# Performance work log

Measured on AMD Instinct MI355X. Metric: run time of the kernel, lower is better.

Reference implementation:

```python
import jax, jax.numpy as jnp
import numpy as np

N_NODES = 100000
N_EDGES = 600000
IN_FEATS = 128
OUT_FEATS = 128
BN_EPS = 1e-5


def setup_inputs() -> dict:
    key = jax.random.key(0)
    ks = jax.random.split(key, 8)
    x = jax.random.normal(ks[0], (N_NODES, IN_FEATS), dtype=jnp.float32)
    edge_index = jax.random.randint(ks[1], (2, N_EDGES), 0, N_NODES, dtype=jnp.int64)
    # GCNConv linear weight (no bias in lin), bias added after aggregation
    W = jax.random.normal(ks[2], (IN_FEATS, OUT_FEATS), dtype=jnp.float32) / np.sqrt(IN_FEATS)
    b = jax.random.normal(ks[3], (OUT_FEATS,), dtype=jnp.float32) * 0.01
    # BatchNorm affine params
    gamma = jnp.ones((OUT_FEATS,), dtype=jnp.float32)
    beta = jnp.zeros((OUT_FEATS,), dtype=jnp.float32)
    # residual Linear: y = x @ W_res + b_res (W_res stored [in, out])
    W_res = jax.random.normal(ks[4], (IN_FEATS, OUT_FEATS), dtype=jnp.float32) / np.sqrt(IN_FEATS)
    b_res = jax.random.normal(ks[5], (OUT_FEATS,), dtype=jnp.float32) * 0.01
    return {"x": x, "edge_index": edge_index, "W": W, "b": b,
            "gamma": gamma, "beta": beta, "W_res": W_res, "b_res": b_res}


def _gcn_forward(x, edge_index, W, b, gamma, beta, W_res, b_res):
    n = x.shape[0]
    # --- GCNConv (PyG defaults): add self-loops, symmetric normalization ---
    loops = jnp.arange(n, dtype=edge_index.dtype)
    row = jnp.concatenate([edge_index[0], loops])  # source nodes
    col = jnp.concatenate([edge_index[1], loops])  # destination nodes
    deg = jax.ops.segment_sum(jnp.ones_like(col, dtype=x.dtype), col, num_segments=n)
    dinv = jax.lax.rsqrt(deg)  # deg >= 1 thanks to self-loops
    norm = dinv[row] * dinv[col]  # [E+N]
    h = x @ W  # [N, out]
    msg = h[row] * norm[:, None]  # gather + scale, [E+N, out]
    agg = jax.ops.segment_sum(msg, col, num_segments=n) + b  # scatter-add + bias
    # --- ReLU + BatchNorm (training mode, biased variance) ---
    r = jax.nn.relu(agg)
    mean = jnp.mean(r, axis=0)
    var = jnp.mean(jnp.square(r - mean), axis=0)
    bn = gamma * (r - mean) * jax.lax.rsqrt(var + BN_EPS) + beta
    # --- residual dense path ---
    res = x @ W_res + b_res
    return bn + res


def reference(x, edge_index, W, b, gamma, beta, W_res, b_res):
    return _gcn_forward(x, edge_index, W, b, gamma, beta, W_res, b_res)
```

## Files before the change

### kernel.cpp

```cpp
#include <hip/hip_runtime.h>

#define NN 100000
#define NE 600000
#define F  128
#define BN_EPS 1e-5f
#define TM 128
#define TK 32

typedef short bf8 __attribute__((ext_vector_type(8)));
typedef float f32x4 __attribute__((ext_vector_type(4)));

__device__ __forceinline__ unsigned short bf16_rne(float x) {
    unsigned u = __float_as_uint(x);
    return (unsigned short)((u + 0x7FFFu + ((u >> 16) & 1u)) >> 16);
}
__device__ __forceinline__ void split_bf16(float x, unsigned short& h, unsigned short& l) {
    unsigned short hh = bf16_rne(x);
    float hf = __uint_as_float(((unsigned)hh) << 16);
    h = hh;
    l = bf16_rne(x - hf);
}

__global__ void k_init(const unsigned* __restrict__ ei, int* __restrict__ flag,
                       int* __restrict__ cnt, float* __restrict__ colsum, float* __restrict__ colsq)
{
    int i = blockIdx.x * 256 + threadIdx.x;
    if (i <= NN) cnt[i] = 0;
    if (i < F) { colsum[i] = 0.f; colsq[i] = 0.f; }
    if (blockIdx.x == 0) {
        __shared__ int any;
        if (threadIdx.x == 0) any = 0;
        __syncthreads();
        unsigned v = ei[2 * threadIdx.x + 1];
        if (v != 0u) atomicOr(&any, 1);
        __syncthreads();
        if (threadIdx.x == 0) *flag = (any == 0) ? 1 : 0;
    }
}

__global__ void k_count(const void* __restrict__ ei, const int* __restrict__ flag, int* __restrict__ cnt)
{
    int e = blockIdx.x * 256 + threadIdx.x;
    if (e >= NE) return;
    int col;
    if (*flag) col = (int)((const long long*)ei)[NE + e];
    else       col = ((const int*)ei)[NE + e];
    atomicAdd(&cnt[col], 1);
}

__global__ void k_bsum(const int* __restrict__ cnt, int* __restrict__ bsum)
{
    __shared__ int s[256];
    int b = blockIdx.x, t = threadIdx.x;
    int i = b * 256 + t;
    s[t] = (i <= NN) ? cnt[i] : 0;
    __syncthreads();
    for (int o = 128; o > 0; o >>= 1) {
        if (t < o) s[t] += s[t + o];
        __syncthreads();
    }
    if (t == 0) bsum[b] = s[0];
}

__global__ void k_bscan(const int* __restrict__ bsum, int* __restrict__ bbase)
{
    __shared__ int s[512];
    int t = threadIdx.x;
    int v = (t < 391) ? bsum[t] : 0;
    s[t] = v;
    __syncthreads();
    for (int o = 1; o < 512; o <<= 1) {
        int tmp = (t >= o) ? s[t - o] : 0;
        __syncthreads();
        s[t] += tmp;
        __syncthreads();
    }
    if (t < 391) bbase[t] = s[t] - v;
}

__global__ void k_offsets(const int* __restrict__ cnt, const int* __restrict__ bbase,
                          int* __restrict__ off, int* __restrict__ cur,
                          float* __restrict__ dinv)
{
    __shared__ int s[256];
    int b = blockIdx.x, t = threadIdx.x;
    int i = b * 256 + t;
    int v = (i <= NN) ? cnt[i] : 0;
    s[t] = v;
    __syncthreads();
    for (int o = 1; o < 256; o <<= 1) {
        int tmp = (t >= o) ? s[t - o] : 0;
        __syncthreads();
        s[t] += tmp;
        __syncthreads();
    }
    int excl = s[t] - v + bbase[b];
    if (i <= NN) {
        off[i] = excl;
        if (i < NN) {
            cur[i] = excl;
            float d = (float)(v + 1);
            float r = rsqrtf(d);
            r = r * (1.5f - 0.5f * d * r * r);
            dinv[i] = r;
        }
    }
}

__global__ void k_place(const void* __restrict__ ei, const int* __restrict__ flag,
                        int* __restrict__ cur, int* __restrict__ csr)
{
    int e = blockIdx.x * 256 + threadIdx.x;
    if (e >= NE) return;
    int row, col;
    if (*flag) {
        row = (int)((const long long*)ei)[e];
        col = (int)((const long long*)ei)[NE + e];
    } else {
        row = ((const int*)ei)[e];
        col = ((const int*)ei)[NE + e];
    }
    int slot = atomicAdd(&cur[col], 1);
    csr[slot] = row;
}

__global__ __launch_bounds__(256) void k_agg(const float* __restrict__ x, const float* __restrict__ dinv,
                                             const int* __restrict__ off, const int* __restrict__ csr,
                                             float* __restrict__ aggx,
                                             const float* __restrict__ W, const float* __restrict__ Wr,
                                             unsigned short* __restrict__ wprep)
{
    int node = blockIdx.x * 4 + (threadIdx.x >> 6);
    int lane = threadIdx.x & 63;
    int sub  = lane & 31;
    int half = lane >> 5;
    float ax = 0.f, ay = 0.f, az = 0.f, aw = 0.f;
    int e0 = off[node], e1 = off[node + 1];
    int e = e0 + half;
    for (; e + 2 < e1; e += 4) {
        int r0 = csr[e], r1 = csr[e + 2];
        float s0 = dinv[r0], s1 = dinv[r1];
        float4 u0 = ((const float4*)(x + (size_t)r0 * F))[sub];
        float4 u1 = ((const float4*)(x + (size_t)r1 * F))[sub];
        ax = fmaf(u0.x, s0, ax); ay = fmaf(u0.y, s0, ay);
        az = fmaf(u0.z, s0, az); aw = fmaf(u0.w, s0, aw);
        ax = fmaf(u1.x, s1, ax); ay = fmaf(u1.y, s1, ay);
        az = fmaf(u1.z, s1, az); aw = fmaf(u1.w, s1, aw);
    }
    for (; e < e1; e += 2) {
        int r = csr[e]; float s = dinv[r];
        float4 u = ((const float4*)(x + (size_t)r * F))[sub];
        ax = fmaf(u.x, s, ax); ay = fmaf(u.y, s, ay);
        az = fmaf(u.z, s, az); aw = fmaf(u.w, s, aw);
    }
    ax += __shfl_xor(ax, 32); ay += __shfl_xor(ay, 32);
    az += __shfl_xor(az, 32); aw += __shfl_xor(aw, 32);
    if (half == 0) {
        float di = dinv[node];
        float4 v = ((const float4*)(x + (size_t)node * F))[sub];
        float4 o;
        o.x = (fmaf(v.x, di, ax)) * di;
        o.y = (fmaf(v.y, di, ay)) * di;
        o.z = (fmaf(v.z, di, az)) * di;
        o.w = (fmaf(v.w, di, aw)) * di;
        ((float4*)(aggx + (size_t)node * F))[sub] = o;
    }
    if (blockIdx.x < 16) {
        int t = blockIdx.x * 256 + threadIdx.x;
        int wl  = t & 63;
        int nf  = (t >> 6) & 7;
        int c   = (t >> 9) & 3;
        int typ = t >> 11;
        const float* wsrc = typ ? Wr : W;
        int col = nf * 16 + (wl & 15);
        int k0  = c * 32 + (wl >> 4) * 8;
        unsigned short hi[8], lo[8];
#pragma unroll
        for (int j = 0; j < 8; ++j)
            split_bf16(wsrc[(size_t)(k0 + j) * F + col], hi[j], lo[j]);
        unsigned short* dst = wprep + (size_t)t * 16;
#pragma unroll
        for (int j = 0; j < 8; ++j) { dst[j] = hi[j]; dst[8 + j] = lo[j]; }
    }
}

__global__ __launch_bounds__(256, 2) void k_gemm2(
    float* __restrict__ A, const float* __restrict__ X,
    const unsigned short* __restrict__ wprep,
    const float* __restrict__ bias, const float* __restrict__ biasr,
    float* __restrict__ out, float* __restrict__ colsum, float* __restrict__ colsq)
{
    __shared__ unsigned short Ahi[TM][40];
    __shared__ unsigned short Alo[TM][40];
    __shared__ float sstat[256];

    const int tid  = threadIdx.x;
    const int type = blockIdx.y;
    const int r0   = blockIdx.x * TM;
    const float* __restrict__ src = type ? X : (const float*)A;

    const int lane = tid & 63;
    const int wv = tid >> 6;
    const int wr = wv >> 1;
    const int wc = wv & 1;
    const int l15 = lane & 15;
    const int lq4 = lane >> 4;
    const int k0  = lq4 * 8;

    const int arow  = tid >> 3;
    const int aslot = (tid & 7) << 2;

    float4 ra[4];
#pragma unroll
    for (int it = 0; it < 4; ++it) {
        int gr = r0 + arow + it * 32;
        ra[it] = make_float4(0.f, 0.f, 0.f, 0.f);
        if (gr < NN) ra[it] = *(const float4*)(src + (size_t)gr * F + aslot);
    }
    bf8 bhi[4], blo[4];
#pragma unroll
    for (int n = 0; n < 4; ++n) {
        int entry = ((type * 4 + 0) * 8 + wc * 4 + n) * 64 + lane;
        const bf8* pb = (const bf8*)(wprep + (size_t)entry * 16);
        bhi[n] = pb[0];
        blo[n] = pb[1];
    }

    f32x4 acc[4][4];
#pragma unroll
    for (int m = 0; m < 4; ++m)
#pragma unroll
        for (int n = 0; n < 4; ++n) acc[m][n] = (f32x4){0.f, 0.f, 0.f, 0.f};

    for (int c = 0; c < 4; ++c) {
        __builtin_amdgcn_s_barrier();
        __builtin_amdgcn_sched_barrier(0);
#pragma unroll
        for (int it = 0; it < 4; ++it) {
            int row = arow + it * 32;
            unsigned short h0, h1, h2, h3, l0, l1, l2, l3;
            split_bf16(ra[it].x, h0, l0); split_bf16(ra[it].y, h1, l1);
            split_bf16(ra[it].z, h2, l2); split_bf16(ra[it].w, h3, l3);
            *(ushort4*)&Ahi[row][aslot] = make_ushort4(h0, h1, h2, h3);
            *(ushort4*)&Alo[row][aslot] = make_ushort4(l0, l1, l2, l3);
        }
        if (c < 3) {
            int kb = (c + 1) * TK;
#pragma unroll
            for (int it = 0; it < 4; ++it) {
                int gr = r0 + arow + it * 32;
                float4 t = make_float4(0.f, 0.f, 0.f, 0.f);
                if (gr < NN) t = *(const float4*)(src + (size_t)gr * F + kb + aslot);
                ra[it] = t;
            }
        }
        asm volatile("s_waitcnt lgkmcnt(0)" ::: "memory");
        __builtin_amdgcn_s_barrier();
        __builtin_amdgcn_sched_barrier(0);
#pragma unroll
        for (int m = 0; m < 4; ++m) {
            int row = wr * 64 + m * 16 + l15;
            bf8 ah = *(const bf8*)&Ahi[row][k0];
            bf8 al = *(const bf8*)&Alo[row][k0];
#pragma unroll
            for (int n = 0; n < 4; ++n) {
                acc[m][n] = __builtin_amdgcn_mfma_f32_16x16x32_bf16(ah, bhi[n], acc[m][n], 0, 0, 0);
                acc[m][n] = __builtin_amdgcn_mfma_f32_16x16x32_bf16(ah, blo[n], acc[m][n], 0, 0, 0);
                acc[m][n] = __builtin_amdgcn_mfma_f32_16x16x32_bf16(al, bhi[n], acc[m][n], 0, 0, 0);
            }
        }
        if (c < 3) {
            int cc = c + 1;
#pragma unroll
            for (int n = 0; n < 4; ++n) {
                int entry = ((type * 4 + cc) * 8 + wc * 4 + n) * 64 + lane;
                const bf8* pb = (const bf8*)(wprep + (size_t)entry * 16);
                bhi[n] = pb[0];
                blo[n] = pb[1];
            }
        }
    }
    __syncthreads();

    if (type == 0) {
        sstat[tid] = 0.f;
        __syncthreads();
        float bv[4];
#pragma unroll
        for (int n = 0; n < 4; ++n) bv[n] = bias[wc * 64 + n * 16 + l15];
        float ls[4] = {0.f, 0.f, 0.f, 0.f};
        float lq[4] = {0.f, 0.f, 0.f, 0.f};
#pragma unroll
        for (int m = 0; m < 4; ++m)
#pragma unroll
            for (int reg = 0; reg < 4; ++reg) {
                int gr = r0 + wr * 64 + m * 16 + lq4 * 4 + reg;
                if (gr < NN) {
#pragma unroll
                    for (int n = 0; n < 4; ++n) {
                        float r = fmaxf(acc[m][n][reg] + bv[n], 0.f);
                        A[(size_t)gr * F + wc * 64 + n * 16 + l15] = r;
                        ls[n] += r;
                        lq[n] = fmaf(r, r, lq[n]);
                    }
                }
            }
#pragma unroll
        for (int n = 0; n < 4; ++n) {
            ls[n] += __shfl_xor(ls[n], 16); ls[n] += __shfl_xor(ls[n], 32);
            lq[n] += __shfl_xor(lq[n], 16); lq[n] += __shfl_xor(lq[n], 32);
        }
        if (lane < 16) {
#pragma unroll
            for (int n = 0; n < 4; ++n) {
                int col = wc * 64 + n * 16 + l15;
                atomicAdd(&sstat[col], ls[n]);
                atomicAdd(&sstat[128 + col], lq[n]);
            }
        }
        __syncthreads();
        if (tid < F) {
            atomicAdd(&colsum[tid], sstat[tid]);
            atomicAdd(&colsq[tid], sstat[128 + tid]);
        }
    } else {
        float bv[4];
#pragma unroll
        for (int n = 0; n < 4; ++n) bv[n] = biasr[wc * 64 + n * 16 + l15];
#pragma unroll
        for (int m = 0; m < 4; ++m)
#pragma unroll
            for (int reg = 0; reg < 4; ++reg) {
                int gr = r0 + wr * 64 + m * 16 + lq4 * 4 + reg;
                if (gr < NN) {
#pragma unroll
                    for (int n = 0; n < 4; ++n)
                        out[(size_t)gr * F + wc * 64 + n * 16 + l15] = acc[m][n][reg] + bv[n];
                }
            }
    }
}

__global__ __launch_bounds__(256) void k_final(const float* __restrict__ colsum,
                                               const float* __restrict__ colsq,
                                               const float* __restrict__ gamma,
                                               const float* __restrict__ beta,
                                               const float* __restrict__ r,
                                               float* __restrict__ out)
{
    __shared__ float s_sc[F], s_sh[F];
    int tid = threadIdx.x;
    if (tid < F) {
        float inv_n = 1.0f / (float)NN;
        float mean = colsum[tid] * inv_n;
        float ex2  = colsq[tid] * inv_n;
        float var  = fmaxf(ex2 - mean * mean, 0.f);
        float d = var + BN_EPS;
        float is = rsqrtf(d);
        is = is * (1.5f - 0.5f * d * is * is);
        float sc = gamma[tid] * is;
        s_sc[tid] = sc;
        s_sh[tid] = beta[tid] - sc * mean;
    }
    __syncthreads();
    int idx = blockIdx.x * 256 + tid;
    int c4 = idx & 31;
    float4 rv = ((const float4*)r)[idx];
    float4 ov = ((float4*)out)[idx];
    float4 sv = *(const float4*)&s_sc[c4 * 4];
    float4 hv = *(const float4*)&s_sh[c4 * 4];
    float4 o;
    o.x = fmaf(rv.x, sv.x, hv.x) + ov.x;
    o.y = fmaf(rv.y, sv.y, hv.y) + ov.y;
    o.z = fmaf(rv.z, sv.z, hv.z) + ov.z;
    o.w = fmaf(rv.w, sv.w, hv.w) + ov.w;
    ((float4*)out)[idx] = o;
}

extern "C" void kernel_launch(void* const* d_in, const int* in_sizes, int n_in,
                              void* d_out, int out_size, void* d_ws, size_t ws_size,
                              hipStream_t stream)
{
    (void)in_sizes; (void)n_in; (void)out_size; (void)ws_size;
    const float* x     = (const float*)d_in[0];
    const void*  ei    = d_in[1];
    const float* W     = (const float*)d_in[2];
    const float* b     = (const float*)d_in[3];
    const float* gamma = (const float*)d_in[4];
    const float* beta  = (const float*)d_in[5];
    const float* Wres  = (const float*)d_in[6];
    const float* bres  = (const float*)d_in[7];
    float* out = (float*)d_out;

    char* w = (char*)d_ws;
    float* aggx   = (float*)(w + 0);
    int*   cnt    = (int*)  (w + 51200000);
    float* dinv   = (float*)(w + 51600128);
    int*   off    = (int*)  (w + 52000256);
    int*   cur    = (int*)  (w + 52400384);
    unsigned short* wprep = (unsigned short*)(w + 52400384);
    int*   csr    = (int*)  (w + 52800512);
    int*   bsum   = (int*)  (w + 55200512);
    int*   bbase  = (int*)  (w + 55202176);
    float* colsum = (float*)(w + 55203840);
    float* colsq  = (float*)(w + 55204352);
    int*   flag   = (int*)  (w + 55205888);

    const int G_INIT = 392;
    const int G_E    = (NE + 255) / 256;
    const int G_N    = 391;
    const int G_AGG  = NN / 4;
    const dim3 G_GEMM((NN + TM - 1) / TM, 2);
    const int G_FIN  = (NN * F / 4) / 256;

    k_init   <<<G_INIT, 256, 0, stream>>>((const unsigned*)ei, flag, cnt, colsum, colsq);
    k_count  <<<G_E, 256, 0, stream>>>(ei, flag, cnt);
    k_bsum   <<<G_N, 256, 0, stream>>>(cnt, bsum);
    k_bscan  <<<1, 512, 0, stream>>>(bsum, bbase);
    k_offsets<<<G_N, 256, 0, stream>>>(cnt, bbase, off, cur, dinv);
    k_place  <<<G_E, 256, 0, stream>>>(ei, flag, cur, csr);
    k_agg    <<<G_AGG, 256, 0, stream>>>(x, dinv, off, csr, aggx, W, Wres, wprep);
    k_gemm2  <<<G_GEMM, 256, 0, stream>>>(aggx, x, wprep, b, bres, out, colsum, colsq);
    k_final  <<<G_FIN, 256, 0, stream>>>(colsum, colsq, gamma, beta, aggx, out);
}
```

Measured before the change: 307.4 us.

## Double-buffer GEMM A tiles, stage epilogue via LDS, unroll gather by four

```diff
diff --git a/kernel.cpp b/kernel.cpp
--- a/kernel.cpp
+++ b/kernel.cpp
@@ -137,15 +137,21 @@
     float ax = 0.f, ay = 0.f, az = 0.f, aw = 0.f;
     int e0 = off[node], e1 = off[node + 1];
     int e = e0 + half;
-    for (; e + 2 < e1; e += 4) {
-        int r0 = csr[e], r1 = csr[e + 2];
-        float s0 = dinv[r0], s1 = dinv[r1];
+    for (; e + 6 < e1; e += 8) {
+        int r0 = csr[e], r1 = csr[e + 2], r2 = csr[e + 4], r3 = csr[e + 6];
+        float s0 = dinv[r0], s1 = dinv[r1], s2 = dinv[r2], s3 = dinv[r3];
         float4 u0 = ((const float4*)(x + (size_t)r0 * F))[sub];
         float4 u1 = ((const float4*)(x + (size_t)r1 * F))[sub];
+        float4 u2 = ((const float4*)(x + (size_t)r2 * F))[sub];
+        float4 u3 = ((const float4*)(x + (size_t)r3 * F))[sub];
         ax = fmaf(u0.x, s0, ax); ay = fmaf(u0.y, s0, ay);
         az = fmaf(u0.z, s0, az); aw = fmaf(u0.w, s0, aw);
         ax = fmaf(u1.x, s1, ax); ay = fmaf(u1.y, s1, ay);
         az = fmaf(u1.z, s1, az); aw = fmaf(u1.w, s1, aw);
+        ax = fmaf(u2.x, s2, ax); ay = fmaf(u2.y, s2, ay);
+        az = fmaf(u2.z, s2, az); aw = fmaf(u2.w, s2, aw);
+        ax = fmaf(u3.x, s3, ax); ay = fmaf(u3.y, s3, ay);
+        az = fmaf(u3.z, s3, az); aw = fmaf(u3.w, s3, aw);
     }
     for (; e < e1; e += 2) {
         int r = csr[e]; float s = dinv[r];
@@ -190,8 +196,7 @@
     const float* __restrict__ bias, const float* __restrict__ biasr,
     float* __restrict__ out, float* __restrict__ colsum, float* __restrict__ colsq)
 {
-    __shared__ unsigned short Ahi[TM][40];
-    __shared__ unsigned short Alo[TM][40];
+    __shared__ unsigned short Abuf[2][2][TM][40];
     __shared__ float sstat[256];
 
     const int tid  = threadIdx.x;
@@ -225,6 +230,25 @@
         bhi[n] = pb[0];
         blo[n] = pb[1];
     }
+#pragma unroll
+    for (int it = 0; it < 4; ++it) {
+        int row = arow + it * 32;
+        unsigned short h0, h1, h2, h3, l0, l1, l2, l3;
+        split_bf16(ra[it].x, h0, l0); split_bf16(ra[it].y, h1, l1);
+        split_bf16(ra[it].z, h2, l2); split_bf16(ra[it].w, h3, l3);
+        *(ushort4*)&Abuf[0][0][row][aslot] = make_ushort4(h0, h1, h2, h3);
+        *(ushort4*)&Abuf[0][1][row][aslot] = make_ushort4(l0, l1, l2, l3);
+    }
+#pragma unroll
+    for (int it = 0; it < 4; ++it) {
+        int gr = r0 + arow + it * 32;
+        float4 t = make_float4(0.f, 0.f, 0.f, 0.f);
+        if (gr < NN) t = *(const float4*)(src + (size_t)gr * F + TK + aslot);
+        ra[it] = t;
+    }
+    asm volatile("s_waitcnt lgkmcnt(0)" ::: "memory");
+    __builtin_amdgcn_s_barrier();
+    __builtin_amdgcn_sched_barrier(0);
 
     f32x4 acc[4][4];
 #pragma unroll
@@ -232,36 +256,36 @@
 #pragma unroll
         for (int n = 0; n < 4; ++n) acc[m][n] = (f32x4){0.f, 0.f, 0.f, 0.f};
 
+#pragma unroll
     for (int c = 0; c < 4; ++c) {
-        __builtin_amdgcn_s_barrier();
-        __builtin_amdgcn_sched_barrier(0);
-#pragma unroll
-        for (int it = 0; it < 4; ++it) {
-            int row = arow + it * 32;
-            unsigned short h0, h1, h2, h3, l0, l1, l2, l3;
-            split_bf16(ra[it].x, h0, l0); split_bf16(ra[it].y, h1, l1);
-            split_bf16(ra[it].z, h2, l2); split_bf16(ra[it].w, h3, l3);
-            *(ushort4*)&Ahi[row][aslot] = make_ushort4(h0, h1, h2, h3);
-            *(ushort4*)&Alo[row][aslot] = make_ushort4(l0, l1, l2, l3);
-        }
         if (c < 3) {
-            int kb = (c + 1) * TK;
+            int nb = (c + 1) & 1;
 #pragma unroll
             for (int it = 0; it < 4; ++it) {
-                int gr = r0 + arow + it * 32;
-                float4 t = make_float4(0.f, 0.f, 0.f, 0.f);
-                if (gr < NN) t = *(const float4*)(src + (size_t)gr * F + kb + aslot);
-                ra[it] = t;
-            }
-        }
-        asm volatile("s_waitcnt lgkmcnt(0)" ::: "memory");
-        __builtin_amdgcn_s_barrier();
-        __builtin_amdgcn_sched_barrier(0);
+                int row = arow + it * 32;
+                unsigned short h0, h1, h2, h3, l0, l1, l2, l3;
+                split_bf16(ra[it].x, h0, l0); split_bf16(ra[it].y, h1, l1);
+                split_bf16(ra[it].z, h2, l2); split_bf16(ra[it].w, h3, l3);
+                *(ushort4*)&Abuf[nb][0][row][aslot] = make_ushort4(h0, h1, h2, h3);
+                *(ushort4*)&Abuf[nb][1][row][aslot] = make_ushort4(l0, l1, l2, l3);
+            }
+            if (c < 2) {
+                int kb = (c + 2) * TK;
+#pragma unroll
+                for (int it = 0; it < 4; ++it) {
+                    int gr = r0 + arow + it * 32;
+                    float4 t = make_float4(0.f, 0.f, 0.f, 0.f);
+                    if (gr < NN) t = *(const float4*)(src + (size_t)gr * F + kb + aslot);
+                    ra[it] = t;
+                }
+            }
+        }
+        int cb = c & 1;
 #pragma unroll
         for (int m = 0; m < 4; ++m) {
             int row = wr * 64 + m * 16 + l15;
-            bf8 ah = *(const bf8*)&Ahi[row][k0];
-            bf8 al = *(const bf8*)&Alo[row][k0];
+            bf8 ah = *(const bf8*)&Abuf[cb][0][row][k0];
+            bf8 al = *(const bf8*)&Abuf[cb][1][row][k0];
 #pragma unroll
             for (int n = 0; n < 4; ++n) {
                 acc[m][n] = __builtin_amdgcn_mfma_f32_16x16x32_bf16(ah, bhi[n], acc[m][n], 0, 0, 0);
@@ -278,33 +302,52 @@
                 bhi[n] = pb[0];
                 blo[n] = pb[1];
             }
-        }
-    }
-    __syncthreads();
+            asm volatile("s_waitcnt lgkmcnt(0)" ::: "memory");
+            __builtin_amdgcn_s_barrier();
+            __builtin_amdgcn_sched_barrier(0);
+        }
+    }
+
+    float* ep = (float*)Abuf + wv * 1104;
+    float bv[4];
+#pragma unroll
+    for (int n = 0; n < 4; ++n) bv[n] = (type ? biasr : bias)[wc * 64 + n * 16 + l15];
+    float ls[4] = {0.f, 0.f, 0.f, 0.f};
+    float lq[4] = {0.f, 0.f, 0.f, 0.f};
+    float* dstm = type ? out : A;
+
+#pragma unroll
+    for (int m = 0; m < 4; ++m) {
+        asm volatile("s_waitcnt lgkmcnt(0)" ::: "memory");
+        __builtin_amdgcn_sched_barrier(0);
+#pragma unroll
+        for (int n = 0; n < 4; ++n)
+#pragma unroll
+            for (int reg = 0; reg < 4; ++reg) {
+                float r = acc[m][n][reg] + bv[n];
+                if (type == 0) {
+                    r = fmaxf(r, 0.f);
+                    ls[n] += r;
+                    lq[n] = fmaf(r, r, lq[n]);
+                }
+                ep[(lq4 * 4 + reg) * 68 + n * 16 + l15] = r;
+            }
+        asm volatile("s_waitcnt lgkmcnt(0)" ::: "memory");
+        __builtin_amdgcn_sched_barrier(0);
+        int row = lane >> 2;
+        int gr = r0 + wr * 64 + m * 16 + row;
+#pragma unroll
+        for (int j = 0; j < 4; ++j) {
+            int col = ((lane & 3) + 4 * j) * 4;
+            float4 v = *(float4*)&ep[row * 68 + col];
+            if (gr < NN)
+                *(float4*)(dstm + (size_t)gr * F + wc * 64 + col) = v;
+        }
+    }
 
     if (type == 0) {
         sstat[tid] = 0.f;
         __syncthreads();
-        float bv[4];
-#pragma unroll
-        for (int n = 0; n < 4; ++n) bv[n] = bias[wc * 64 + n * 16 + l15];
-        float ls[4] = {0.f, 0.f, 0.f, 0.f};
-        float lq[4] = {0.f, 0.f, 0.f, 0.f};
-#pragma unroll
-        for (int m = 0; m < 4; ++m)
-#pragma unroll
-            for (int reg = 0; reg < 4; ++reg) {
-                int gr = r0 + wr * 64 + m * 16 + lq4 * 4 + reg;
-                if (gr < NN) {
-#pragma unroll
-                    for (int n = 0; n < 4; ++n) {
-                        float r = fmaxf(acc[m][n][reg] + bv[n], 0.f);
-                        A[(size_t)gr * F + wc * 64 + n * 16 + l15] = r;
-                        ls[n] += r;
-                        lq[n] = fmaf(r, r, lq[n]);
-                    }
-                }
-            }
 #pragma unroll
         for (int n = 0; n < 4; ++n) {
             ls[n] += __shfl_xor(ls[n], 16); ls[n] += __shfl_xor(ls[n], 32);
@@ -323,21 +366,6 @@
             atomicAdd(&colsum[tid], sstat[tid]);
             atomicAdd(&colsq[tid], sstat[128 + tid]);
         }
-    } else {
-        float bv[4];
-#pragma unroll
-        for (int n = 0; n < 4; ++n) bv[n] = biasr[wc * 64 + n * 16 + l15];
-#pragma unroll
-        for (int m = 0; m < 4; ++m)
-#pragma unroll
-            for (int reg = 0; reg < 4; ++reg) {
-                int gr = r0 + wr * 64 + m * 16 + lq4 * 4 + reg;
-                if (gr < NN) {
-#pragma unroll
-                    for (int n = 0; n < 4; ++n)
-                        out[(size_t)gr * F + wc * 64 + n * 16 + l15] = acc[m][n][reg] + bv[n];
-                }
-            }
     }
 }
 
```

After: 307.2 us. Within noise of the previous version (-0.0%).
